# Kernel optimization log

Measured on AMD Instinct MI355X. Metric: run time of the kernel, lower is better.

Reference implementation:

```python
import jax, jax.numpy as jnp
import numpy as np

M, N = 2048, 128  # m basis operators, n-dim Hilbert space

def setup_inputs() -> dict:
    key = jax.random.key(0)
    k1, k2, k3, k4 = jax.random.split(key, 4)
    return {
        "basis_re": jax.random.normal(k1, (M, N, N), dtype=jnp.float32),
        "basis_im": jax.random.normal(k2, (M, N, N), dtype=jnp.float32),
        "theta": jax.random.uniform(k3, (4, N), dtype=jnp.float32, minval=-1.0, maxval=1.0),
        "evl": jax.random.uniform(k4, (2,), dtype=jnp.float32, minval=-1.0, maxval=1.0),
    }

def reference(basis_re, basis_im, theta, evl):
    m = basis_re.shape[0]
    # basis_orth_conj: conj of basis, flattened to (m, n*n)
    B = (basis_re - 1j * basis_im).reshape(m, -1)
    # first eigenvector
    c0 = theta[0] + 1j * theta[1]
    evc0 = c0 / jnp.linalg.norm(c0)
    # second eigenvector, Gram-Schmidt against evc0 (vdot conjugates 1st arg)
    c1 = theta[2] + 1j * theta[3]
    c1 = c1 - jnp.vdot(evc0, c1) * evc0
    evc1 = c1 / jnp.linalg.norm(c1)
    # eigenvalues: softplus then L2-normalize
    lam = jax.nn.softplus(evl)
    lam = lam / jnp.linalg.norm(lam)
    # rank-2 Hermitian: lam0 * evc0 evc0^H - lam1 * evc1 evc1^H  (n, n)
    matH = evc0[:, None] * (evc0.conj() * lam[0]) - evc1[:, None] * (evc1.conj() * lam[1])
    # (m, n^2) @ (n^2,) complex matvec, then squared L2 norm
    v = B @ matH.reshape(-1)
    return jnp.sum((v.conj() * v).real)
```

## Files before the change

### kernel.cpp

```cpp
#include <hip/hip_runtime.h>
#include <hip/hip_bf16.h>

#define N 128
#define NN (N * N)
#define M 2048

__device__ __forceinline__ float block_reduce128(float v, float* red, int i) {
    __syncthreads();
    red[i] = v;
    __syncthreads();
    for (int off = 64; off > 0; off >>= 1) {
        if (i < off) red[i] += red[i + off];
        __syncthreads();
    }
    return red[0];
}

__global__ void prep_kernel(const float* __restrict__ theta,
                            const float* __restrict__ evl,
                            float* __restrict__ H) {
    __shared__ float e0r[N], e0i[N], e1r[N], e1i[N];
    __shared__ float red[N];
    __shared__ float s_lam0, s_lam1;
    const int i = threadIdx.x;

    float c0r = theta[i], c0i = theta[N + i];
    float s0 = block_reduce128(c0r * c0r + c0i * c0i, red, i);
    float inv0 = rsqrtf(s0);
    float a0r = c0r * inv0, a0i = c0i * inv0;
    e0r[i] = a0r; e0i[i] = a0i;

    float c1r = theta[2 * N + i], c1i = theta[3 * N + i];
    float dr = block_reduce128(a0r * c1r + a0i * c1i, red, i);
    float di = block_reduce128(a0r * c1i - a0i * c1r, red, i);
    c1r -= dr * a0r - di * a0i;
    c1i -= dr * a0i + di * a0r;

    float s1 = block_reduce128(c1r * c1r + c1i * c1i, red, i);
    float inv1 = rsqrtf(s1);
    float a1r = c1r * inv1, a1i = c1i * inv1;
    e1r[i] = a1r; e1i[i] = a1i;

    if (i == 0) {
        float l0 = log1pf(expf(evl[0]));
        float l1 = log1pf(expf(evl[1]));
        float inl = rsqrtf(l0 * l0 + l1 * l1);
        s_lam0 = l0 * inl;
        s_lam1 = l1 * inl;
    }
    __syncthreads();
    const float lam0 = s_lam0, lam1 = s_lam1;

    for (int j = 0; j < N; ++j) {
        float c0rj = e0r[j], c0ij = e0i[j];
        float c1rj = e1r[j], c1ij = e1i[j];
        float hr = lam0 * (a0r * c0rj + a0i * c0ij)
                 - lam1 * (a1r * c1rj + a1i * c1ij);
        float hi = lam0 * (a0i * c0rj - a0r * c0ij)
                 - lam1 * (a1i * c1rj - a1r * c1ij);
        H[i * N + j]      = hr;
        H[NN + i * N + j] = hi;
    }
}

__global__ __launch_bounds__(256) void main_kernel(
        const float4* __restrict__ br, const float4* __restrict__ bi,
        const float4* __restrict__ H, float* __restrict__ out) {
    const int k = blockIdx.x;
    const int t = threadIdx.x;
    const float4* brk = br + (size_t)k * (NN / 4);
    const float4* bik = bi + (size_t)k * (NN / 4);
    const float4* Hr = H;
    const float4* Hi = H + (NN / 4);

    float vr = 0.f, vi = 0.f;
    #pragma unroll 4
    for (int it = t; it < NN / 4; it += 256) {
        float4 a  = brk[it];
        float4 b  = bik[it];
        float4 hr = Hr[it];
        float4 hi = Hi[it];
        vr += a.x * hr.x + b.x * hi.x;  vi += a.x * hi.x - b.x * hr.x;
        vr += a.y * hr.y + b.y * hi.y;  vi += a.y * hi.y - b.y * hr.y;
        vr += a.z * hr.z + b.z * hi.z;  vi += a.z * hi.z - b.z * hr.z;
        vr += a.w * hr.w + b.w * hi.w;  vi += a.w * hi.w - b.w * hr.w;
    }

    for (int off = 32; off > 0; off >>= 1) {
        vr += __shfl_down(vr, off);
        vi += __shfl_down(vi, off);
    }
    __shared__ float swr[4], swi[4];
    const int wave = t >> 6, lane = t & 63;
    if (lane == 0) { swr[wave] = vr; swi[wave] = vi; }
    __syncthreads();
    if (t == 0) {
        float R = swr[0] + swr[1] + swr[2] + swr[3];
        float I = swi[0] + swi[1] + swi[2] + swi[3];
        atomicAdd(out, R * R + I * I);
    }
}

extern "C" void kernel_launch(void* const* d_in, const int* in_sizes, int n_in,
                              void* d_out, int out_size, void* d_ws, size_t ws_size,
                              hipStream_t stream) {
    const float* basis_re = (const float*)d_in[0];
    const float* basis_im = (const float*)d_in[1];
    const float* theta    = (const float*)d_in[2];
    const float* evl      = (const float*)d_in[3];
    float* out = (float*)d_out;
    float* H   = (float*)d_ws;

    hipMemsetAsync(d_out, 0, sizeof(float), stream);
    prep_kernel<<<1, 128, 0, stream>>>(theta, evl, H);
    main_kernel<<<M, 256, 0, stream>>>((const float4*)basis_re,
                                       (const float4*)basis_im,
                                       (const float4*)H, out);
}
```

Before: 292.5 us.

## Recompute rank-2 H on the fly from eigenvectors in shared memory

The prep kernel now writes only the two eigenvectors and the eigenvalues instead of materialising the full 128x128 complex H matrix. Each main-kernel block stages those 514 floats into LDS and rebuilds the H entries in registers, so blocks no longer read H from global memory alongside the basis. The main loop is fully unrolled with software prefetch of the next basis float4s, and launch bounds request higher occupancy. The trade is extra ALU work per element and LDS reads, in exchange for removing half of the per-block memory reads.

```diff
diff --git a/kernel.cpp b/kernel.cpp
--- a/kernel.cpp
+++ b/kernel.cpp
@@ -1,5 +1,4 @@
 #include <hip/hip_runtime.h>
-#include <hip/hip_bf16.h>
 
 #define N 128
 #define NN (N * N)
@@ -18,17 +17,14 @@
 
 __global__ void prep_kernel(const float* __restrict__ theta,
                             const float* __restrict__ evl,
-                            float* __restrict__ H) {
-    __shared__ float e0r[N], e0i[N], e1r[N], e1i[N];
+                            float* __restrict__ ws) {
     __shared__ float red[N];
-    __shared__ float s_lam0, s_lam1;
     const int i = threadIdx.x;
 
     float c0r = theta[i], c0i = theta[N + i];
     float s0 = block_reduce128(c0r * c0r + c0i * c0i, red, i);
     float inv0 = rsqrtf(s0);
     float a0r = c0r * inv0, a0i = c0i * inv0;
-    e0r[i] = a0r; e0i[i] = a0i;
 
     float c1r = theta[2 * N + i], c1i = theta[3 * N + i];
     float dr = block_reduce128(a0r * c1r + a0i * c1i, red, i);
@@ -39,58 +35,82 @@
     float s1 = block_reduce128(c1r * c1r + c1i * c1i, red, i);
     float inv1 = rsqrtf(s1);
     float a1r = c1r * inv1, a1i = c1i * inv1;
-    e1r[i] = a1r; e1i[i] = a1i;
 
+    ws[i]         = a0r;
+    ws[N + i]     = a0i;
+    ws[2 * N + i] = a1r;
+    ws[3 * N + i] = a1i;
     if (i == 0) {
         float l0 = log1pf(expf(evl[0]));
         float l1 = log1pf(expf(evl[1]));
         float inl = rsqrtf(l0 * l0 + l1 * l1);
-        s_lam0 = l0 * inl;
-        s_lam1 = l1 * inl;
-    }
-    __syncthreads();
-    const float lam0 = s_lam0, lam1 = s_lam1;
-
-    for (int j = 0; j < N; ++j) {
-        float c0rj = e0r[j], c0ij = e0i[j];
-        float c1rj = e1r[j], c1ij = e1i[j];
-        float hr = lam0 * (a0r * c0rj + a0i * c0ij)
-                 - lam1 * (a1r * c1rj + a1i * c1ij);
-        float hi = lam0 * (a0i * c0rj - a0r * c0ij)
-                 - lam1 * (a1i * c1rj - a1r * c1ij);
-        H[i * N + j]      = hr;
-        H[NN + i * N + j] = hi;
+        ws[4 * N]     = l0 * inl;
+        ws[4 * N + 1] = l1 * inl;
     }
 }
 
-__global__ __launch_bounds__(256) void main_kernel(
+#define COMP(comp)                                                   \
+    {                                                                \
+        float x0r = e0ri * E0r.comp + e0ii * E0i.comp;               \
+        float x0i = e0ii * E0r.comp - e0ri * E0i.comp;               \
+        float x1r = e1ri * E1r.comp + e1ii * E1i.comp;               \
+        float x1i = e1ii * E1r.comp - e1ri * E1i.comp;               \
+        float hr = lam0 * x0r - lam1 * x1r;                          \
+        float hi = lam0 * x0i - lam1 * x1i;                          \
+        vr += a.comp * hr + b.comp * hi;                             \
+        vi += a.comp * hi - b.comp * hr;                             \
+    }
+
+__global__ __launch_bounds__(256, 8) void main_kernel(
         const float4* __restrict__ br, const float4* __restrict__ bi,
-        const float4* __restrict__ H, float* __restrict__ out) {
+        const float* __restrict__ ws, float* __restrict__ out) {
+    __shared__ __align__(16) float le[4 * N];
+    __shared__ float slam[2];
+    __shared__ float swr[4], swi[4];
+    const int t = threadIdx.x;
     const int k = blockIdx.x;
-    const int t = threadIdx.x;
+
+    if (t < 128) {
+        le[t]       = ws[t];
+        le[t + 128] = ws[t + 128];
+        le[t + 256] = ws[t + 256];
+        le[t + 384] = ws[t + 384];
+    }
+    if (t < 2) slam[t] = ws[512 + t];
+    __syncthreads();
+    const float lam0 = slam[0], lam1 = slam[1];
+    const float4* e0r4 = (const float4*)(le);
+    const float4* e0i4 = (const float4*)(le + 128);
+    const float4* e1r4 = (const float4*)(le + 256);
+    const float4* e1i4 = (const float4*)(le + 384);
+
     const float4* brk = br + (size_t)k * (NN / 4);
     const float4* bik = bi + (size_t)k * (NN / 4);
-    const float4* Hr = H;
-    const float4* Hi = H + (NN / 4);
 
     float vr = 0.f, vi = 0.f;
-    #pragma unroll 4
-    for (int it = t; it < NN / 4; it += 256) {
-        float4 a  = brk[it];
-        float4 b  = bik[it];
-        float4 hr = Hr[it];
-        float4 hi = Hi[it];
-        vr += a.x * hr.x + b.x * hi.x;  vi += a.x * hi.x - b.x * hr.x;
-        vr += a.y * hr.y + b.y * hi.y;  vi += a.y * hi.y - b.y * hr.y;
-        vr += a.z * hr.z + b.z * hi.z;  vi += a.z * hi.z - b.z * hr.z;
-        vr += a.w * hr.w + b.w * hi.w;  vi += a.w * hi.w - b.w * hr.w;
+    float4 a0 = brk[t];
+    float4 b0 = bik[t];
+    #pragma unroll
+    for (int c = 0; c < 16; ++c) {
+        float4 a = a0, b = b0;
+        if (c < 15) {
+            a0 = brk[t + 256 * (c + 1)];
+            b0 = bik[t + 256 * (c + 1)];
+        }
+        const int it = t + 256 * c;
+        const int i  = it >> 5;
+        const int j4 = it & 31;
+        const float e0ri = le[i],       e0ii = le[128 + i];
+        const float e1ri = le[256 + i], e1ii = le[384 + i];
+        const float4 E0r = e0r4[j4], E0i = e0i4[j4];
+        const float4 E1r = e1r4[j4], E1i = e1i4[j4];
+        COMP(x) COMP(y) COMP(z) COMP(w)
     }
 
     for (int off = 32; off > 0; off >>= 1) {
         vr += __shfl_down(vr, off);
         vi += __shfl_down(vi, off);
     }
-    __shared__ float swr[4], swi[4];
     const int wave = t >> 6, lane = t & 63;
     if (lane == 0) { swr[wave] = vr; swi[wave] = vi; }
     __syncthreads();
@@ -109,11 +129,11 @@
     const float* theta    = (const float*)d_in[2];
     const float* evl      = (const float*)d_in[3];
     float* out = (float*)d_out;
-    float* H   = (float*)d_ws;
+    float* ws  = (float*)d_ws;
 
     hipMemsetAsync(d_out, 0, sizeof(float), stream);
-    prep_kernel<<<1, 128, 0, stream>>>(theta, evl, H);
+    prep_kernel<<<1, 128, 0, stream>>>(theta, evl, ws);
     main_kernel<<<M, 256, 0, stream>>>((const float4*)basis_re,
                                        (const float4*)basis_im,
-                                       (const float4*)H, out);
+                                       ws, out);
 }
```

Measured after the change: 286.0 us. 1.02x faster.

## Exploit rank-2 structure of H instead of materializing dense matrix

Applied to the files above, without the earlier changes.

The prep kernel no longer builds the dense 128x128 complex H. It stores only the two normalized eigenvectors and their lambda-scaled copies. Each wave now handles one real or imaginary basis slice and computes the contraction as a bilinear form through the eigenvectors, which removes the per-block streaming of H. The dot kernel adds a register prefetch ring for the basis loads, and a separate reduce kernel combines the partial products. This trades H bandwidth and L2 traffic for more FLOPs per element plus one extra kernel launch.

```diff
diff --git a/kernel.cpp b/kernel.cpp
--- a/kernel.cpp
+++ b/kernel.cpp
@@ -1,9 +1,9 @@
 #include <hip/hip_runtime.h>
-#include <hip/hip_bf16.h>
 
 #define N 128
-#define NN (N * N)
+#define NN 16384
 #define M 2048
+
 
 __device__ __forceinline__ float block_reduce128(float v, float* red, int i) {
     __syncthreads();
@@ -18,17 +18,14 @@
 
 __global__ void prep_kernel(const float* __restrict__ theta,
                             const float* __restrict__ evl,
-                            float* __restrict__ H) {
-    __shared__ float e0r[N], e0i[N], e1r[N], e1i[N];
+                            float* __restrict__ ws) {
     __shared__ float red[N];
-    __shared__ float s_lam0, s_lam1;
     const int i = threadIdx.x;
 
     float c0r = theta[i], c0i = theta[N + i];
     float s0 = block_reduce128(c0r * c0r + c0i * c0i, red, i);
     float inv0 = rsqrtf(s0);
     float a0r = c0r * inv0, a0i = c0i * inv0;
-    e0r[i] = a0r; e0i[i] = a0i;
 
     float c1r = theta[2 * N + i], c1i = theta[3 * N + i];
     float dr = block_reduce128(a0r * c1r + a0i * c1i, red, i);
@@ -39,66 +36,93 @@
     float s1 = block_reduce128(c1r * c1r + c1i * c1i, red, i);
     float inv1 = rsqrtf(s1);
     float a1r = c1r * inv1, a1i = c1i * inv1;
-    e1r[i] = a1r; e1i[i] = a1i;
 
-    if (i == 0) {
-        float l0 = log1pf(expf(evl[0]));
-        float l1 = log1pf(expf(evl[1]));
-        float inl = rsqrtf(l0 * l0 + l1 * l1);
-        s_lam0 = l0 * inl;
-        s_lam1 = l1 * inl;
-    }
-    __syncthreads();
-    const float lam0 = s_lam0, lam1 = s_lam1;
+    float l0 = log1pf(expf(evl[0]));
+    float l1 = log1pf(expf(evl[1]));
+    float inl = rsqrtf(l0 * l0 + l1 * l1);
+    l0 *= inl; l1 *= inl;
 
-    for (int j = 0; j < N; ++j) {
-        float c0rj = e0r[j], c0ij = e0i[j];
-        float c1rj = e1r[j], c1ij = e1i[j];
-        float hr = lam0 * (a0r * c0rj + a0i * c0ij)
-                 - lam1 * (a1r * c1rj + a1i * c1ij);
-        float hi = lam0 * (a0i * c0rj - a0r * c0ij)
-                 - lam1 * (a1i * c1rj - a1r * c1ij);
-        H[i * N + j]      = hr;
-        H[NN + i * N + j] = hi;
-    }
+    float4* E4 = (float4*)ws;
+    E4[i]       = make_float4(a0r, a0i, a1r, a1i);
+    E4[128 + i] = make_float4(l0 * a0r, l0 * a0i, l1 * a1r, l1 * a1i);
 }
 
-__global__ __launch_bounds__(256) void main_kernel(
+__global__ __launch_bounds__(256, 4) void dot_kernel(
         const float4* __restrict__ br, const float4* __restrict__ bi,
-        const float4* __restrict__ H, float* __restrict__ out) {
-    const int k = blockIdx.x;
+        const float* __restrict__ ws, float2* __restrict__ jout) {
+    __shared__ __align__(16) float4 sG[N];
     const int t = threadIdx.x;
-    const float4* brk = br + (size_t)k * (NN / 4);
-    const float4* bik = bi + (size_t)k * (NN / 4);
-    const float4* Hr = H;
-    const float4* Hi = H + (NN / 4);
+    if (t < N) sG[t] = ((const float4*)ws)[N + t];
 
-    float vr = 0.f, vi = 0.f;
-    #pragma unroll 4
-    for (int it = t; it < NN / 4; it += 256) {
-        float4 a  = brk[it];
-        float4 b  = bik[it];
-        float4 hr = Hr[it];
-        float4 hi = Hi[it];
-        vr += a.x * hr.x + b.x * hi.x;  vi += a.x * hi.x - b.x * hr.x;
-        vr += a.y * hr.y + b.y * hi.y;  vi += a.y * hi.y - b.y * hr.y;
-        vr += a.z * hr.z + b.z * hi.z;  vi += a.z * hi.z - b.z * hr.z;
-        vr += a.w * hr.w + b.w * hi.w;  vi += a.w * hi.w - b.w * hr.w;
+    const int lane = t & 63;
+    const int wave = t >> 6;
+    const int job  = blockIdx.x * 4 + wave;
+    const int k    = job >> 1;
+    const float4* __restrict__ src =
+        ((job & 1) ? bi : br) + (size_t)k * (NN / 4);
+
+    const int j4 = lane & 31;
+    const float4* E4 = (const float4*)ws;
+    float4 E0 = E4[4 * j4 + 0];
+    float4 E1 = E4[4 * j4 + 1];
+    float4 E2 = E4[4 * j4 + 2];
+    float4 E3 = E4[4 * j4 + 3];
+    const int h = lane >> 5;
+    __syncthreads();
+
+    float4 buf[4];
+    #pragma unroll
+    for (int p = 0; p < 4; ++p) buf[p] = src[64 * p + lane];
+
+    float P = 0.f, Q = 0.f;
+
+#define BODY(a, c)                                                        \
+    {                                                                     \
+        float4 g = sG[2 * (c) + h];                                       \
+        float d0r = a.x * E0.x + a.y * E1.x + a.z * E2.x + a.w * E3.x;    \
+        float d0i = a.x * E0.y + a.y * E1.y + a.z * E2.y + a.w * E3.y;    \
+        float d1r = a.x * E0.z + a.y * E1.z + a.z * E2.z + a.w * E3.z;    \
+        float d1i = a.x * E0.w + a.y * E1.w + a.z * E2.w + a.w * E3.w;    \
+        P += g.x * d0r + g.y * d0i - g.z * d1r - g.w * d1i;               \
+        Q += g.y * d0r - g.x * d0i - g.w * d1r + g.z * d1i;               \
     }
 
+    int c = 0;
+    #pragma unroll 4
+    for (; c < 60; ++c) {
+        float4 a = buf[c & 3];
+        buf[c & 3] = src[64 * (c + 4) + lane];
+        BODY(a, c)
+    }
+    #pragma unroll
+    for (; c < 64; ++c) {
+        float4 a = buf[c & 3];
+        BODY(a, c)
+    }
+#undef BODY
+
     for (int off = 32; off > 0; off >>= 1) {
-        vr += __shfl_down(vr, off);
-        vi += __shfl_down(vi, off);
+        P += __shfl_down(P, off);
+        Q += __shfl_down(Q, off);
     }
-    __shared__ float swr[4], swi[4];
-    const int wave = t >> 6, lane = t & 63;
-    if (lane == 0) { swr[wave] = vr; swi[wave] = vi; }
+    if (lane == 0) jout[job] = make_float2(P, Q);
+}
+
+__global__ __launch_bounds__(256) void reduce_kernel(
+        const float4* __restrict__ jout4, float* __restrict__ out) {
+    const int k = blockIdx.x * 256 + threadIdx.x;
+    float4 f = jout4[k];
+    float vr = f.x + f.w;
+    float vi = f.y - f.z;
+    float s = vr * vr + vi * vi;
+
+    for (int off = 32; off > 0; off >>= 1) s += __shfl_down(s, off);
+    __shared__ float sw[4];
+    const int wave = threadIdx.x >> 6, lane = threadIdx.x & 63;
+    if (lane == 0) sw[wave] = s;
     __syncthreads();
-    if (t == 0) {
-        float R = swr[0] + swr[1] + swr[2] + swr[3];
-        float I = swi[0] + swi[1] + swi[2] + swi[3];
-        atomicAdd(out, R * R + I * I);
-    }
+    if (threadIdx.x == 0)
+        atomicAdd(out, sw[0] + sw[1] + sw[2] + sw[3]);
 }
 
 extern "C" void kernel_launch(void* const* d_in, const int* in_sizes, int n_in,
@@ -109,11 +133,12 @@
     const float* theta    = (const float*)d_in[2];
     const float* evl      = (const float*)d_in[3];
     float* out = (float*)d_out;
-    float* H   = (float*)d_ws;
+    float* ws  = (float*)d_ws;
 
     hipMemsetAsync(d_out, 0, sizeof(float), stream);
-    prep_kernel<<<1, 128, 0, stream>>>(theta, evl, H);
-    main_kernel<<<M, 256, 0, stream>>>((const float4*)basis_re,
-                                       (const float4*)basis_im,
-                                       (const float4*)H, out);
+    prep_kernel<<<1, 128, 0, stream>>>(theta, evl, ws);
+    dot_kernel<<<M / 2, 256, 0, stream>>>((const float4*)basis_re,
+                                          (const float4*)basis_im,
+                                          ws, (float2*)(ws + 1024));
+    reduce_kernel<<<8, 256, 0, stream>>>((const float4*)(ws + 1024), out);
 }
```

Result: no change. 290.7 us (-0.6%).

## Exploit rank-2 structure of H and stream basis tiles via direct-to-LDS loads

Applied to the files above, without the earlier changes.

The prep kernel no longer materializes the full 128x128 complex H matrix. It writes only the two eigenvectors and their eigenvalue-scaled copies, and the dot kernel computes each basis row's contraction with the eigenvectors and then combines rows with the scaled vectors. Basis data is streamed tile by tile into LDS with global_load_lds, four buffers deep and two tiles ahead, with one barrier per tile. This removes the H reads (128 KB per block from cache), but the kernel now does 32 block-wide synchronizations per block and depends on the async LDS load path.

```diff
diff --git a/kernel.cpp b/kernel.cpp
--- a/kernel.cpp
+++ b/kernel.cpp
@@ -1,9 +1,19 @@
 #include <hip/hip_runtime.h>
-#include <hip/hip_bf16.h>
 
 #define N 128
-#define NN (N * N)
+#define NN 16384
 #define M 2048
+#define TILE_F4 256
+#define TPS 16
+#define TOT 32
+
+
+__device__ __forceinline__ void gl_lds16(const float4* g, float4* l) {
+    __builtin_amdgcn_global_load_lds(
+        (__attribute__((address_space(1))) void*)const_cast<float4*>(g),
+        (__attribute__((address_space(3))) void*)l,
+        16, 0, 0);
+}
 
 __device__ __forceinline__ float block_reduce128(float v, float* red, int i) {
     __syncthreads();
@@ -18,17 +28,14 @@
 
 __global__ void prep_kernel(const float* __restrict__ theta,
                             const float* __restrict__ evl,
-                            float* __restrict__ H) {
-    __shared__ float e0r[N], e0i[N], e1r[N], e1i[N];
+                            float* __restrict__ ws) {
     __shared__ float red[N];
-    __shared__ float s_lam0, s_lam1;
     const int i = threadIdx.x;
 
     float c0r = theta[i], c0i = theta[N + i];
     float s0 = block_reduce128(c0r * c0r + c0i * c0i, red, i);
     float inv0 = rsqrtf(s0);
     float a0r = c0r * inv0, a0i = c0i * inv0;
-    e0r[i] = a0r; e0i[i] = a0i;
 
     float c1r = theta[2 * N + i], c1i = theta[3 * N + i];
     float dr = block_reduce128(a0r * c1r + a0i * c1i, red, i);
@@ -39,58 +46,69 @@
     float s1 = block_reduce128(c1r * c1r + c1i * c1i, red, i);
     float inv1 = rsqrtf(s1);
     float a1r = c1r * inv1, a1i = c1i * inv1;
-    e1r[i] = a1r; e1i[i] = a1i;
 
-    if (i == 0) {
-        float l0 = log1pf(expf(evl[0]));
-        float l1 = log1pf(expf(evl[1]));
-        float inl = rsqrtf(l0 * l0 + l1 * l1);
-        s_lam0 = l0 * inl;
-        s_lam1 = l1 * inl;
-    }
-    __syncthreads();
-    const float lam0 = s_lam0, lam1 = s_lam1;
+    float l0 = log1pf(expf(evl[0]));
+    float l1 = log1pf(expf(evl[1]));
+    float inl = rsqrtf(l0 * l0 + l1 * l1);
+    l0 *= inl; l1 *= inl;
 
-    for (int j = 0; j < N; ++j) {
-        float c0rj = e0r[j], c0ij = e0i[j];
-        float c1rj = e1r[j], c1ij = e1i[j];
-        float hr = lam0 * (a0r * c0rj + a0i * c0ij)
-                 - lam1 * (a1r * c1rj + a1i * c1ij);
-        float hi = lam0 * (a0i * c0rj - a0r * c0ij)
-                 - lam1 * (a1i * c1rj - a1r * c1ij);
-        H[i * N + j]      = hr;
-        H[NN + i * N + j] = hi;
-    }
+    float4* E4 = (float4*)ws;
+    E4[i]       = make_float4(a0r, a0i, a1r, a1i);
+    E4[128 + i] = make_float4(l0 * a0r, l0 * a0i, l1 * a1r, l1 * a1i);
 }
 
-__global__ __launch_bounds__(256) void main_kernel(
+__global__ __launch_bounds__(256, 8) void dot_kernel(
         const float4* __restrict__ br, const float4* __restrict__ bi,
-        const float4* __restrict__ H, float* __restrict__ out) {
+        const float* __restrict__ ws, float* __restrict__ out) {
+    __shared__ __align__(16) float4 stage[4][TILE_F4];
+    __shared__ __align__(16) float4 sG[N];
+    __shared__ float swr[4], swi[4];
+    const int t = threadIdx.x;
     const int k = blockIdx.x;
-    const int t = threadIdx.x;
-    const float4* brk = br + (size_t)k * (NN / 4);
-    const float4* bik = bi + (size_t)k * (NN / 4);
-    const float4* Hr = H;
-    const float4* Hi = H + (NN / 4);
 
-    float vr = 0.f, vi = 0.f;
-    #pragma unroll 4
-    for (int it = t; it < NN / 4; it += 256) {
-        float4 a  = brk[it];
-        float4 b  = bik[it];
-        float4 hr = Hr[it];
-        float4 hi = Hi[it];
-        vr += a.x * hr.x + b.x * hi.x;  vi += a.x * hi.x - b.x * hr.x;
-        vr += a.y * hr.y + b.y * hi.y;  vi += a.y * hi.y - b.y * hr.y;
-        vr += a.z * hr.z + b.z * hi.z;  vi += a.z * hi.z - b.z * hr.z;
-        vr += a.w * hr.w + b.w * hi.w;  vi += a.w * hi.w - b.w * hr.w;
+    if (t < N) sG[t] = ((const float4*)ws)[N + t];
+
+    const float4* E4 = (const float4*)ws;
+    const int j4 = t & 31;
+    float4 E0 = E4[4 * j4 + 0];
+    float4 E1 = E4[4 * j4 + 1];
+    float4 E2 = E4[4 * j4 + 2];
+    float4 E3 = E4[4 * j4 + 3];
+
+    const float4* srcR = br + (size_t)k * (NN / 4);
+    const float4* srcI = bi + (size_t)k * (NN / 4);
+
+    gl_lds16(srcR + 0 * TILE_F4 + t, &stage[0][t]);
+    gl_lds16(srcR + 1 * TILE_F4 + t, &stage[1][t]);
+
+    float Pr = 0.f, Qr = 0.f, Pi = 0.f, Qi = 0.f;
+    for (int tt = 0; tt < TOT; ++tt) {
+        if (tt < TOT - 2) {
+            const int nt = tt + 2;
+            const float4* s = (nt < TPS) ? (srcR + nt * TILE_F4)
+                                         : (srcI + (nt - TPS) * TILE_F4);
+            gl_lds16(s + t, &stage[nt & 3][t]);
+        }
+        __syncthreads();
+
+        float4 a = stage[tt & 3][t];
+        const int row = ((tt & 15) << 3) + (t >> 5);
+        float4 g = sG[row];
+        float d0r = a.x * E0.x + a.y * E1.x + a.z * E2.x + a.w * E3.x;
+        float d0i = a.x * E0.y + a.y * E1.y + a.z * E2.y + a.w * E3.y;
+        float d1r = a.x * E0.z + a.y * E1.z + a.z * E2.z + a.w * E3.z;
+        float d1i = a.x * E0.w + a.y * E1.w + a.z * E2.w + a.w * E3.w;
+        float dP = g.x * d0r + g.y * d0i - g.z * d1r - g.w * d1i;
+        float dQ = g.y * d0r - g.x * d0i - g.w * d1r + g.z * d1i;
+        if (tt < TPS) { Pr += dP; Qr += dQ; }
+        else          { Pi += dP; Qi += dQ; }
     }
 
+    float vr = Pr + Qi, vi = Qr - Pi;
     for (int off = 32; off > 0; off >>= 1) {
         vr += __shfl_down(vr, off);
         vi += __shfl_down(vi, off);
     }
-    __shared__ float swr[4], swi[4];
     const int wave = t >> 6, lane = t & 63;
     if (lane == 0) { swr[wave] = vr; swi[wave] = vi; }
     __syncthreads();
@@ -109,11 +127,11 @@
     const float* theta    = (const float*)d_in[2];
     const float* evl      = (const float*)d_in[3];
     float* out = (float*)d_out;
-    float* H   = (float*)d_ws;
+    float* ws  = (float*)d_ws;
 
     hipMemsetAsync(d_out, 0, sizeof(float), stream);
-    prep_kernel<<<1, 128, 0, stream>>>(theta, evl, H);
-    main_kernel<<<M, 256, 0, stream>>>((const float4*)basis_re,
-                                       (const float4*)basis_im,
-                                       (const float4*)H, out);
+    prep_kernel<<<1, 128, 0, stream>>>(theta, evl, ws);
+    dot_kernel<<<M, 256, 0, stream>>>((const float4*)basis_re,
+                                      (const float4*)basis_im,
+                                      ws, out);
 }
```

Result: no change. 294.4 us (+0.7%).
